# Kernel tuning notes

Measured on AMD Instinct MI355X. Metric: run time of the kernel, lower is better.

Reference implementation:

```python
import jax, jax.numpy as jnp
import numpy as np

N_NODES = 50000
N_EDGES = 800000
HEADS = 8
DIM = 32
NEG_SLOPE = 0.2


def setup_inputs() -> dict:
    key = jax.random.key(0)
    k1, k2, k3, k4, k5 = jax.random.split(key, 5)
    feat = jax.random.normal(k1, (N_NODES, HEADS * DIM), dtype=jnp.float32)
    attn_l = jax.random.normal(k2, (1, HEADS, DIM), dtype=jnp.float32)
    attn_r = jax.random.normal(k3, (1, HEADS, DIM), dtype=jnp.float32)
    src_idx = jax.random.randint(k4, (N_EDGES,), 0, N_NODES, dtype=jnp.int32)
    dst_idx = jnp.sort(jax.random.randint(k5, (N_EDGES,), 0, N_NODES, dtype=jnp.int32))
    return {"feat": feat, "attn_l": attn_l, "attn_r": attn_r,
            "src_idx": src_idx, "dst_idx": dst_idx}


def reference(feat, attn_l, attn_r, src_idx, dst_idx):
    # [N, H, D] node features
    h = feat.reshape(-1, HEADS, DIM)
    n = h.shape[0]
    # per-node attention logits: [N, H]
    el = jnp.sum(h * attn_l, axis=-1)
    er = jnp.sum(h * attn_r, axis=-1)
    # edge scores e = leaky_relu(el[u] + er[v]): [E, H]
    e = jax.nn.leaky_relu(el[src_idx] + er[dst_idx], negative_slope=NEG_SLOPE)
    # segment softmax over incoming edges of each dst node
    e_max = jax.ops.segment_max(e, dst_idx, num_segments=n)          # [N, H]
    e_exp = jnp.exp(e - e_max[dst_idx])                              # [E, H]
    denom = jax.ops.segment_sum(e_exp, dst_idx, num_segments=n)     # [N, H]
    a = e_exp / denom[dst_idx]                                      # [E, H]
    # weighted scatter-sum aggregation: sum_{u in N(v)} a_uv * h_u
    m = h[src_idx] * a[:, :, None]                                  # [E, H, D]
    out = jax.ops.segment_sum(m, dst_idx, num_segments=n)           # [N, H, D]
    return out
```

## Files before the change

### kernel.cpp

```cpp
#include <hip/hip_runtime.h>
#include <hip/hip_fp16.h>
#include <math.h>

#define HEADS 8
#define DIM 32
#define NEG_SLOPE 0.2f

__device__ inline float2 u2f2(unsigned int u) {
    __half2 h = __builtin_bit_cast(__half2, u);
    return __half22float2(h);
}

__global__ __launch_bounds__(256) void gat_prep_kernel(
    const float4* __restrict__ feat4,
    const float4* __restrict__ attn_l4,
    const float4* __restrict__ attn_r4,
    float* __restrict__ el,
    float* __restrict__ er,
    uint2* __restrict__ feat_h2,
    const int* __restrict__ dst,
    int* __restrict__ rowptr,
    int n_nodes, int n_edges, int nb_logits) {
    int b = blockIdx.x;
    if (b < nb_logits) {
        int wid = (b * 256 + threadIdx.x) >> 6;
        if (wid >= n_nodes) return;
        int lane = threadIdx.x & 63;
        int h = lane >> 3;
        int q = lane & 7;

        float4 al = attn_l4[lane];
        float4 ar = attn_r4[lane];
        float4 v  = feat4[(size_t)wid * 64 + lane];

        float sl = v.x * al.x + v.y * al.y + v.z * al.z + v.w * al.w;
        float sr = v.x * ar.x + v.y * ar.y + v.z * ar.z + v.w * ar.w;
#pragma unroll
        for (int off = 1; off < 8; off <<= 1) {
            sl += __shfl_xor(sl, off, 64);
            sr += __shfl_xor(sr, off, 64);
        }
        if (q == 0) {
            el[wid * HEADS + h] = sl;
            er[wid * HEADS + h] = sr;
        }
        uint2 o;
        o.x = __builtin_bit_cast(unsigned int, __floats2half2_rn(v.x, v.y));
        o.y = __builtin_bit_cast(unsigned int, __floats2half2_rn(v.z, v.w));
        feat_h2[(size_t)wid * 64 + lane] = o;
    } else {
        int e = (b - nb_logits) * 256 + threadIdx.x;
        if (e >= n_edges) return;
        int d = dst[e];
        int prev = (e > 0) ? dst[e - 1] : -1;
        for (int v = prev + 1; v <= d; ++v) rowptr[v] = e;
        if (e == n_edges - 1) {
            for (int v = d + 1; v <= n_nodes; ++v) rowptr[v] = n_edges;
        }
    }
}

__global__ __launch_bounds__(256) void gat_aggregate_kernel(
    const uint2* __restrict__ feat_h,
    const float* __restrict__ el,
    const float* __restrict__ er,
    const int* __restrict__ src_idx,
    const int* __restrict__ rowptr,
    float4* __restrict__ out4,
    int n_nodes, int total_waves) {
    int wave0 = (blockIdx.x * blockDim.x + threadIdx.x) >> 6;
    int lane = threadIdx.x & 63;
    int h = lane >> 3;

    for (int vraw = wave0; vraw < n_nodes; vraw += total_waves) {
        int v = __builtin_amdgcn_readfirstlane(vraw);
        int start = __builtin_amdgcn_readfirstlane(rowptr[v]);
        int end   = __builtin_amdgcn_readfirstlane(rowptr[v + 1]);

        unsigned obase = ((unsigned)v << 6) + (unsigned)lane;
        if (start == end) {
            out4[obase] = make_float4(0.f, 0.f, 0.f, 0.f);
            continue;
        }
        int endm1 = end - 1;
        float er_vh = er[((unsigned)v << 3) + h];

        float denomA = 0.f, denomB = 0.f;
        float4 acc0 = make_float4(0.f, 0.f, 0.f, 0.f);
        float4 acc1 = make_float4(0.f, 0.f, 0.f, 0.f);

        for (int e = start; e < end; e += 8) {
            int   idx[8];
            uint2 fr[8];
            float elv[8];
#pragma unroll
            for (int i = 0; i < 8; ++i) {
                int ee = (e + i < endm1) ? (e + i) : endm1;
                idx[i] = src_idx[ee];
            }
#pragma unroll
            for (int i = 0; i < 8; ++i) {
                fr[i] = feat_h[((unsigned)idx[i] << 6) + (unsigned)lane];
            }
#pragma unroll
            for (int i = 0; i < 8; ++i) {
                elv[i] = el[((unsigned)idx[i] << 3) + (unsigned)h];
            }
#pragma unroll
            for (int i = 0; i < 8; ++i) {
                float s = elv[i] + er_vh;
                s = fmaxf(s, NEG_SLOPE * s);
                if (e + i > endm1) s = -INFINITY;
                float w = __expf(s);
                float2 lo = u2f2(fr[i].x);
                float2 hi = u2f2(fr[i].y);
                if (i & 1) {
                    denomB += w;
                    acc1.x += w * lo.x; acc1.y += w * lo.y;
                    acc1.z += w * hi.x; acc1.w += w * hi.y;
                } else {
                    denomA += w;
                    acc0.x += w * lo.x; acc0.y += w * lo.y;
                    acc0.z += w * hi.x; acc0.w += w * hi.y;
                }
            }
        }
        float inv = 1.f / (denomA + denomB);
        float4 r;
        r.x = (acc0.x + acc1.x) * inv;
        r.y = (acc0.y + acc1.y) * inv;
        r.z = (acc0.z + acc1.z) * inv;
        r.w = (acc0.w + acc1.w) * inv;
        out4[obase] = r;
    }
}

extern "C" void kernel_launch(void* const* d_in, const int* in_sizes, int n_in,
                              void* d_out, int out_size, void* d_ws, size_t ws_size,
                              hipStream_t stream) {
    const float* feat   = (const float*)d_in[0];
    const float* attn_l = (const float*)d_in[1];
    const float* attn_r = (const float*)d_in[2];
    const int*   src    = (const int*)d_in[3];
    const int*   dst    = (const int*)d_in[4];
    float* out = (float*)d_out;

    int n_edges = in_sizes[3];
    int n_nodes = out_size / (HEADS * DIM);
    int nh = n_nodes * HEADS;

    char* ws = (char*)d_ws;
    float* el = (float*)ws;                       ws += (size_t)nh * 4;
    float* er = (float*)ws;                       ws += (size_t)nh * 4;
    int* rowptr = (int*)ws;                       ws += (size_t)(n_nodes + 1) * 4;
    ws = (char*)(((uintptr_t)ws + 15) & ~(uintptr_t)15);
    uint2* feat_h2 = (uint2*)ws;

    int nb_logits = (n_nodes + 3) / 4;
    int nb_rowptr = (n_edges + 255) / 256;
    hipLaunchKernelGGL(gat_prep_kernel,
                       dim3(nb_logits + nb_rowptr), dim3(256), 0, stream,
                       (const float4*)feat, (const float4*)attn_l,
                       (const float4*)attn_r, el, er, feat_h2,
                       dst, rowptr, n_nodes, n_edges, nb_logits);

    int blocks = 2048;
    int total_waves = blocks * 4;
    hipLaunchKernelGGL(gat_aggregate_kernel,
                       dim3(blocks), dim3(256), 0, stream,
                       (const uint2*)feat_h2, el, er, src, rowptr, (float4*)out,
                       n_nodes, total_waves);
}
```

Measured before the change: 101.7 us.

## Store features and logits head-major and aggregate one head per block

The prep kernel now writes the fp16 features and the el/er logits in a head-major layout. The aggregate kernel launches one block per (4-node group, head) instead of a persistent grid-stride loop. Each wave splits its 64 lanes into four 16-lane groups that each gather a different edge's 64-byte head slice, then combines the groups with cross-lane shuffles and writes with non-temporal stores. The aim is to make each head's gather table small and contiguous for cache reuse. In exchange, src_idx and rowptr are read once per head, gathers become much smaller, and each wave has fewer bytes in flight per iteration.

Result: slower. 180.1 us (+77.0%).

```diff
diff --git a/kernel.cpp b/kernel.cpp
--- a/kernel.cpp
+++ b/kernel.cpp
@@ -5,6 +5,8 @@
 #define HEADS 8
 #define DIM 32
 #define NEG_SLOPE 0.2f
+
+typedef float f32x2 __attribute__((ext_vector_type(2)));
 
 __device__ inline float2 u2f2(unsigned int u) {
     __half2 h = __builtin_bit_cast(__half2, u);
@@ -15,9 +17,9 @@
     const float4* __restrict__ feat4,
     const float4* __restrict__ attn_l4,
     const float4* __restrict__ attn_r4,
-    float* __restrict__ el,
-    float* __restrict__ er,
-    uint2* __restrict__ feat_h2,
+    float* __restrict__ el_ph,
+    float* __restrict__ er_ph,
+    uint2* __restrict__ feat_ph2,
     const int* __restrict__ dst,
     int* __restrict__ rowptr,
     int n_nodes, int n_edges, int nb_logits) {
@@ -40,14 +42,15 @@
             sl += __shfl_xor(sl, off, 64);
             sr += __shfl_xor(sr, off, 64);
         }
+        unsigned hN = (unsigned)h * (unsigned)n_nodes;
         if (q == 0) {
-            el[wid * HEADS + h] = sl;
-            er[wid * HEADS + h] = sr;
+            el_ph[hN + wid] = sl;
+            er_ph[hN + wid] = sr;
         }
         uint2 o;
         o.x = __builtin_bit_cast(unsigned int, __floats2half2_rn(v.x, v.y));
         o.y = __builtin_bit_cast(unsigned int, __floats2half2_rn(v.z, v.w));
-        feat_h2[(size_t)wid * 64 + lane] = o;
+        feat_ph2[((size_t)hN + (unsigned)wid) * 8 + q] = o;
     } else {
         int e = (b - nb_logits) * 256 + threadIdx.x;
         if (e >= n_edges) return;
@@ -61,77 +64,76 @@
 }
 
 __global__ __launch_bounds__(256) void gat_aggregate_kernel(
-    const uint2* __restrict__ feat_h,
-    const float* __restrict__ el,
-    const float* __restrict__ er,
+    const unsigned int* __restrict__ feat_ph,
+    const float* __restrict__ el_ph,
+    const float* __restrict__ er_ph,
     const int* __restrict__ src_idx,
     const int* __restrict__ rowptr,
-    float4* __restrict__ out4,
-    int n_nodes, int total_waves) {
-    int wave0 = (blockIdx.x * blockDim.x + threadIdx.x) >> 6;
+    f32x2* __restrict__ out2,
+    int n_nodes) {
+    int b = blockIdx.x;
+    int h = b & 7;
+    int vraw = (b >> 3) * 4 + (threadIdx.x >> 6);
+    if (vraw >= n_nodes) return;
+    int v = __builtin_amdgcn_readfirstlane(vraw);
     int lane = threadIdx.x & 63;
-    int h = lane >> 3;
+    int grp = lane >> 4;
+    int ql  = lane & 15;
 
-    for (int vraw = wave0; vraw < n_nodes; vraw += total_waves) {
-        int v = __builtin_amdgcn_readfirstlane(vraw);
-        int start = __builtin_amdgcn_readfirstlane(rowptr[v]);
-        int end   = __builtin_amdgcn_readfirstlane(rowptr[v + 1]);
+    int start = __builtin_amdgcn_readfirstlane(rowptr[v]);
+    int end   = __builtin_amdgcn_readfirstlane(rowptr[v + 1]);
 
-        unsigned obase = ((unsigned)v << 6) + (unsigned)lane;
-        if (start == end) {
-            out4[obase] = make_float4(0.f, 0.f, 0.f, 0.f);
-            continue;
+    unsigned ob = ((unsigned)v << 7) + ((unsigned)h << 4) + (unsigned)ql;
+    if (start == end) {
+        if (grp == 0) {
+            f32x2 z; z.x = 0.f; z.y = 0.f;
+            __builtin_nontemporal_store(z, &out2[ob]);
         }
-        int endm1 = end - 1;
-        float er_vh = er[((unsigned)v << 3) + h];
+        return;
+    }
+    int endm1 = end - 1;
+    unsigned hN = (unsigned)h * (unsigned)n_nodes;
+    float er_vh = er_ph[hN + (unsigned)v];
 
-        float denomA = 0.f, denomB = 0.f;
-        float4 acc0 = make_float4(0.f, 0.f, 0.f, 0.f);
-        float4 acc1 = make_float4(0.f, 0.f, 0.f, 0.f);
+    float accx0 = 0.f, accy0 = 0.f, den0 = 0.f;
+    float accx1 = 0.f, accy1 = 0.f, den1 = 0.f;
 
-        for (int e = start; e < end; e += 8) {
-            int   idx[8];
-            uint2 fr[8];
-            float elv[8];
-#pragma unroll
-            for (int i = 0; i < 8; ++i) {
-                int ee = (e + i < endm1) ? (e + i) : endm1;
-                idx[i] = src_idx[ee];
-            }
-#pragma unroll
-            for (int i = 0; i < 8; ++i) {
-                fr[i] = feat_h[((unsigned)idx[i] << 6) + (unsigned)lane];
-            }
-#pragma unroll
-            for (int i = 0; i < 8; ++i) {
-                elv[i] = el[((unsigned)idx[i] << 3) + (unsigned)h];
-            }
-#pragma unroll
-            for (int i = 0; i < 8; ++i) {
-                float s = elv[i] + er_vh;
-                s = fmaxf(s, NEG_SLOPE * s);
-                if (e + i > endm1) s = -INFINITY;
-                float w = __expf(s);
-                float2 lo = u2f2(fr[i].x);
-                float2 hi = u2f2(fr[i].y);
-                if (i & 1) {
-                    denomB += w;
-                    acc1.x += w * lo.x; acc1.y += w * lo.y;
-                    acc1.z += w * hi.x; acc1.w += w * hi.y;
-                } else {
-                    denomA += w;
-                    acc0.x += w * lo.x; acc0.y += w * lo.y;
-                    acc0.z += w * hi.x; acc0.w += w * hi.y;
-                }
-            }
-        }
-        float inv = 1.f / (denomA + denomB);
-        float4 r;
-        r.x = (acc0.x + acc1.x) * inv;
-        r.y = (acc0.y + acc1.y) * inv;
-        r.z = (acc0.z + acc1.z) * inv;
-        r.w = (acc0.w + acc1.w) * inv;
-        out4[obase] = r;
+    for (int e0 = start; e0 < end; e0 += 8) {
+        int eA = e0 + grp;
+        int eB = e0 + 4 + grp;
+        int eeA = eA < endm1 ? eA : endm1;
+        int eeB = eB < endm1 ? eB : endm1;
+        int uA = __builtin_nontemporal_load(&src_idx[eeA]);
+        int uB = __builtin_nontemporal_load(&src_idx[eeB]);
+        unsigned int fA = feat_ph[((size_t)hN + (unsigned)uA) * 16 + ql];
+        unsigned int fB = feat_ph[((size_t)hN + (unsigned)uB) * 16 + ql];
+        float elA = el_ph[hN + (unsigned)uA];
+        float elB = el_ph[hN + (unsigned)uB];
+        float sA = elA + er_vh; sA = fmaxf(sA, NEG_SLOPE * sA);
+        float sB = elB + er_vh; sB = fmaxf(sB, NEG_SLOPE * sB);
+        if (eA > endm1) sA = -INFINITY;
+        if (eB > endm1) sB = -INFINITY;
+        float wA = __expf(sA);
+        float wB = __expf(sB);
+        float2 pA = u2f2(fA);
+        float2 pB = u2f2(fB);
+        den0 += wA; den1 += wB;
+        accx0 += wA * pA.x; accy0 += wA * pA.y;
+        accx1 += wB * pB.x; accy1 += wB * pB.y;
+    }
+    float accx = accx0 + accx1;
+    float accy = accy0 + accy1;
+    float den  = den0 + den1;
+    accx += __shfl_xor(accx, 16, 64);
+    accy += __shfl_xor(accy, 16, 64);
+    den  += __shfl_xor(den,  16, 64);
+    accx += __shfl_xor(accx, 32, 64);
+    accy += __shfl_xor(accy, 32, 64);
+    den  += __shfl_xor(den,  32, 64);
+    if (grp == 0) {
+        float inv = 1.f / den;
+        f32x2 r; r.x = accx * inv; r.y = accy * inv;
+        __builtin_nontemporal_store(r, &out2[ob]);
     }
 }
 
@@ -150,24 +152,23 @@
     int nh = n_nodes * HEADS;
 
     char* ws = (char*)d_ws;
-    float* el = (float*)ws;                       ws += (size_t)nh * 4;
-    float* er = (float*)ws;                       ws += (size_t)nh * 4;
+    float* el_ph = (float*)ws;                    ws += (size_t)nh * 4;
+    float* er_ph = (float*)ws;                    ws += (size_t)nh * 4;
     int* rowptr = (int*)ws;                       ws += (size_t)(n_nodes + 1) * 4;
     ws = (char*)(((uintptr_t)ws + 15) & ~(uintptr_t)15);
-    uint2* feat_h2 = (uint2*)ws;
+    uint2* feat_ph2 = (uint2*)ws;
 
     int nb_logits = (n_nodes + 3) / 4;
     int nb_rowptr = (n_edges + 255) / 256;
     hipLaunchKernelGGL(gat_prep_kernel,
                        dim3(nb_logits + nb_rowptr), dim3(256), 0, stream,
                        (const float4*)feat, (const float4*)attn_l,
-                       (const float4*)attn_r, el, er, feat_h2,
+                       (const float4*)attn_r, el_ph, er_ph, feat_ph2,
                        dst, rowptr, n_nodes, n_edges, nb_logits);
 
-    int blocks = 2048;
-    int total_waves = blocks * 4;
+    int blocks = 8 * ((n_nodes + 3) / 4);
     hipLaunchKernelGGL(gat_aggregate_kernel,
                        dim3(blocks), dim3(256), 0, stream,
-                       (const uint2*)feat_h2, el, er, src, rowptr, (float4*)out,
-                       n_nodes, total_waves);
+                       (const unsigned int*)feat_ph2, el_ph, er_ph, src, rowptr,
+                       (f32x2*)out, n_nodes);
 }
```

## Precompute bf16 edge attention weights in separate pass before aggregation

Applied to the files above, without the earlier changes.

Adds a kernel that computes the exponentiated edge scores once per edge and head, stores them as bf16 in edge order, and writes per-node inverse denominators. The aggregation kernel then reads these weights contiguously instead of gathering el per source and evaluating exp, and it switches to one node per wave with nontemporal stores. The aim is to take the exp and the scattered el gathers out of the bandwidth-bound gather loop. In exchange it adds a third launch, an extra write and read of about 12.8 MB of edge weights, and bf16 rounding of the weights.

After: 110.2 us. 1.08x slower.

```diff
diff --git a/kernel.cpp b/kernel.cpp
--- a/kernel.cpp
+++ b/kernel.cpp
@@ -6,17 +6,28 @@
 #define DIM 32
 #define NEG_SLOPE 0.2f
 
+typedef float f32x4 __attribute__((ext_vector_type(4)));
+
 __device__ inline float2 u2f2(unsigned int u) {
     __half2 h = __builtin_bit_cast(__half2, u);
     return __half22float2(h);
+}
+__device__ inline unsigned short f2bf(float f) {
+    unsigned int u = __builtin_bit_cast(unsigned int, f);
+    u += 0x7FFFu + ((u >> 16) & 1u);
+    return (unsigned short)(u >> 16);
+}
+__device__ inline float bf2f(unsigned short b) {
+    unsigned int u = ((unsigned int)b) << 16;
+    return __builtin_bit_cast(float, u);
 }
 
 __global__ __launch_bounds__(256) void gat_prep_kernel(
     const float4* __restrict__ feat4,
     const float4* __restrict__ attn_l4,
     const float4* __restrict__ attn_r4,
-    float* __restrict__ el,
-    float* __restrict__ er,
+    float* __restrict__ el_n,
+    float* __restrict__ er_n,
     uint2* __restrict__ feat_h2,
     const int* __restrict__ dst,
     int* __restrict__ rowptr,
@@ -41,8 +52,8 @@
             sr += __shfl_xor(sr, off, 64);
         }
         if (q == 0) {
-            el[wid * HEADS + h] = sl;
-            er[wid * HEADS + h] = sr;
+            el_n[(unsigned)wid * 8 + h] = sl;
+            er_n[(unsigned)wid * 8 + h] = sr;
         }
         uint2 o;
         o.x = __builtin_bit_cast(unsigned int, __floats2half2_rn(v.x, v.y));
@@ -60,79 +71,111 @@
     }
 }
 
+__global__ __launch_bounds__(256) void gat_wprep_kernel(
+    const float* __restrict__ el_n,
+    const float* __restrict__ er_n,
+    const int* __restrict__ src_idx,
+    const int* __restrict__ rowptr,
+    unsigned short* __restrict__ w_e,
+    float* __restrict__ inv_den,
+    int n_nodes) {
+    int vraw = (blockIdx.x * blockDim.x + threadIdx.x) >> 6;
+    if (vraw >= n_nodes) return;
+    int v = __builtin_amdgcn_readfirstlane(vraw);
+    int lane = threadIdx.x & 63;
+    int s = lane >> 3;
+    int h = lane & 7;
+
+    int start = __builtin_amdgcn_readfirstlane(rowptr[v]);
+    int end   = __builtin_amdgcn_readfirstlane(rowptr[v + 1]);
+    if (start == end) return;
+
+    float er_vh = er_n[(unsigned)v * 8 + h];
+
+    float den = 0.f;
+    for (int e0 = start; e0 < end; e0 += 8) {
+        int e = e0 + s;
+        int ee = e < end ? e : (end - 1);
+        int u = src_idx[ee];
+        float sc = el_n[(unsigned)u * 8 + h] + er_vh;
+        sc = fmaxf(sc, NEG_SLOPE * sc);
+        float w = __expf(sc);
+        unsigned short wb = f2bf(w);
+        float wf = bf2f(wb);
+        if (e < end) {
+            w_e[(size_t)e * 8 + h] = wb;
+            den += wf;
+        }
+    }
+    den += __shfl_xor(den, 8, 64);
+    den += __shfl_xor(den, 16, 64);
+    den += __shfl_xor(den, 32, 64);
+    if (s == 0) {
+        inv_den[(unsigned)v * 8 + h] = 1.f / den;
+    }
+}
+
 __global__ __launch_bounds__(256) void gat_aggregate_kernel(
     const uint2* __restrict__ feat_h,
-    const float* __restrict__ el,
-    const float* __restrict__ er,
+    const unsigned short* __restrict__ w_e,
+    const float* __restrict__ inv_den,
     const int* __restrict__ src_idx,
     const int* __restrict__ rowptr,
-    float4* __restrict__ out4,
-    int n_nodes, int total_waves) {
-    int wave0 = (blockIdx.x * blockDim.x + threadIdx.x) >> 6;
+    f32x4* __restrict__ out4,
+    int n_nodes) {
+    int vraw = (blockIdx.x * blockDim.x + threadIdx.x) >> 6;
+    if (vraw >= n_nodes) return;
+    int v = __builtin_amdgcn_readfirstlane(vraw);
     int lane = threadIdx.x & 63;
     int h = lane >> 3;
 
-    for (int vraw = wave0; vraw < n_nodes; vraw += total_waves) {
-        int v = __builtin_amdgcn_readfirstlane(vraw);
-        int start = __builtin_amdgcn_readfirstlane(rowptr[v]);
-        int end   = __builtin_amdgcn_readfirstlane(rowptr[v + 1]);
-
-        unsigned obase = ((unsigned)v << 6) + (unsigned)lane;
-        if (start == end) {
-            out4[obase] = make_float4(0.f, 0.f, 0.f, 0.f);
-            continue;
-        }
-        int endm1 = end - 1;
-        float er_vh = er[((unsigned)v << 3) + h];
-
-        float denomA = 0.f, denomB = 0.f;
-        float4 acc0 = make_float4(0.f, 0.f, 0.f, 0.f);
-        float4 acc1 = make_float4(0.f, 0.f, 0.f, 0.f);
-
-        for (int e = start; e < end; e += 8) {
-            int   idx[8];
-            uint2 fr[8];
-            float elv[8];
-#pragma unroll
-            for (int i = 0; i < 8; ++i) {
-                int ee = (e + i < endm1) ? (e + i) : endm1;
-                idx[i] = src_idx[ee];
+    int start = __builtin_amdgcn_readfirstlane(rowptr[v]);
+    int end   = __builtin_amdgcn_readfirstlane(rowptr[v + 1]);
+
+    unsigned obase = ((unsigned)v << 6) + (unsigned)lane;
+    if (start == end) {
+        f32x4 z = {0.f, 0.f, 0.f, 0.f};
+        __builtin_nontemporal_store(z, &out4[obase]);
+        return;
+    }
+    int endm1 = end - 1;
+
+    f32x4 acc0 = {0.f, 0.f, 0.f, 0.f};
+    f32x4 acc1 = {0.f, 0.f, 0.f, 0.f};
+
+    for (int e = start; e < end; e += 8) {
+        int   idx[8];
+        uint2 fr[8];
+        float wv[8];
+#pragma unroll
+        for (int i = 0; i < 8; ++i) {
+            int ee = (e + i < endm1) ? (e + i) : endm1;
+            idx[i] = src_idx[ee];
+            wv[i]  = bf2f(w_e[(size_t)ee * 8 + h]);
+            if (e + i > endm1) wv[i] = 0.f;
+        }
+#pragma unroll
+        for (int i = 0; i < 8; ++i) {
+            fr[i] = feat_h[((unsigned)idx[i] << 6) + (unsigned)lane];
+        }
+#pragma unroll
+        for (int i = 0; i < 8; ++i) {
+            float w = wv[i];
+            float2 lo = u2f2(fr[i].x);
+            float2 hi = u2f2(fr[i].y);
+            if (i & 1) {
+                acc1.x += w * lo.x; acc1.y += w * lo.y;
+                acc1.z += w * hi.x; acc1.w += w * hi.y;
+            } else {
+                acc0.x += w * lo.x; acc0.y += w * lo.y;
+                acc0.z += w * hi.x; acc0.w += w * hi.y;
             }
-#pragma unroll
-            for (int i = 0; i < 8; ++i) {
-                fr[i] = feat_h[((unsigned)idx[i] << 6) + (unsigned)lane];
-            }
-#pragma unroll
-            for (int i = 0; i < 8; ++i) {
-                elv[i] = el[((unsigned)idx[i] << 3) + (unsigned)h];
-            }
-#pragma unroll
-            for (int i = 0; i < 8; ++i) {
-                float s = elv[i] + er_vh;
-                s = fmaxf(s, NEG_SLOPE * s);
-                if (e + i > endm1) s = -INFINITY;
-                float w = __expf(s);
-                float2 lo = u2f2(fr[i].x);
-                float2 hi = u2f2(fr[i].y);
-                if (i & 1) {
-                    denomB += w;
-                    acc1.x += w * lo.x; acc1.y += w * lo.y;
-                    acc1.z += w * hi.x; acc1.w += w * hi.y;
-                } else {
-                    denomA += w;
-                    acc0.x += w * lo.x; acc0.y += w * lo.y;
-                    acc0.z += w * hi.x; acc0.w += w * hi.y;
-                }
-            }
-        }
-        float inv = 1.f / (denomA + denomB);
-        float4 r;
-        r.x = (acc0.x + acc1.x) * inv;
-        r.y = (acc0.y + acc1.y) * inv;
-        r.z = (acc0.z + acc1.z) * inv;
-        r.w = (acc0.w + acc1.w) * inv;
-        out4[obase] = r;
-    }
+        }
+    }
+    float invd = inv_den[((unsigned)v << 3) + (unsigned)h];
+    f32x4 r = acc0 + acc1;
+    r.x *= invd; r.y *= invd; r.z *= invd; r.w *= invd;
+    __builtin_nontemporal_store(r, &out4[obase]);
 }
 
 extern "C" void kernel_launch(void* const* d_in, const int* in_sizes, int n_in,
@@ -150,24 +193,28 @@
     int nh = n_nodes * HEADS;
 
     char* ws = (char*)d_ws;
-    float* el = (float*)ws;                       ws += (size_t)nh * 4;
-    float* er = (float*)ws;                       ws += (size_t)nh * 4;
+    float* el_n = (float*)ws;                     ws += (size_t)nh * 4;
+    float* er_n = (float*)ws;                     ws += (size_t)nh * 4;
+    float* inv_den = (float*)ws;                  ws += (size_t)nh * 4;
     int* rowptr = (int*)ws;                       ws += (size_t)(n_nodes + 1) * 4;
     ws = (char*)(((uintptr_t)ws + 15) & ~(uintptr_t)15);
-    uint2* feat_h2 = (uint2*)ws;
+    uint2* feat_h2 = (uint2*)ws;                  ws += (size_t)nh * 64;
+    unsigned short* w_e = (unsigned short*)ws;
 
     int nb_logits = (n_nodes + 3) / 4;
     int nb_rowptr = (n_edges + 255) / 256;
     hipLaunchKernelGGL(gat_prep_kernel,
                        dim3(nb_logits + nb_rowptr), dim3(256), 0, stream,
                        (const float4*)feat, (const float4*)attn_l,
-                       (const float4*)attn_r, el, er, feat_h2,
+                       (const float4*)attn_r, el_n, er_n, feat_h2,
                        dst, rowptr, n_nodes, n_edges, nb_logits);
 
-    int blocks = 2048;
-    int total_waves = blocks * 4;
+    hipLaunchKernelGGL(gat_wprep_kernel,
+                       dim3((n_nodes + 3) / 4), dim3(256), 0, stream,
+                       el_n, er_n, src, rowptr, w_e, inv_den, n_nodes);
+
     hipLaunchKernelGGL(gat_aggregate_kernel,
-                       dim3(blocks), dim3(256), 0, stream,
-                       (const uint2*)feat_h2, el, er, src, rowptr, (float4*)out,
-                       n_nodes, total_waves);
-}
+                       dim3((n_nodes + 3) / 4), dim3(256), 0, stream,
+                       feat_h2, w_e, inv_den, src, rowptr, (f32x4*)out,
+                       n_nodes);
+}
```
